# Performance work log

Hardware: AMD Instinct MI355X
Metric: run time of the kernel (lower is better)

Reference implementation:

```python
import jax, jax.numpy as jnp
import numpy as np

# Llama-7B FFN up-proj quantized with HQQ 4-bit, group_size=64, axis=0
OUT, IN, GS = 11008, 4096, 64
G = OUT * IN // GS  # 704512 groups


def setup_inputs() -> dict:
    key = jax.random.key(0)
    k1, k2, k3, k4, k5 = jax.random.split(key, 5)
    # packed 4-bit weights: two nibbles per byte, shape [GS//2, G]
    W_q = jax.random.randint(k1, (GS // 2, G), 0, 256, dtype=jnp.int32)
    # per-group scale (meta['scale'] = 1/scale from quantize) and zero
    scale = jax.random.uniform(k2, (1, G), jnp.float32, minval=1e-3, maxval=1e-2)
    zero = jax.random.uniform(k3, (1, G), jnp.float32, minval=0.0, maxval=15.0)
    # decode-style activations: 8 sequences, 1 token each
    x = jax.random.normal(k4, (8, 1, IN), dtype=jnp.float32)
    bias = jax.random.normal(k5, (OUT,), dtype=jnp.float32) * 0.01
    return {"W_q": W_q, "scale": scale, "zero": zero, "x": x, "bias": bias}


def reference(W_q, scale, zero, x, bias):
    # BitPack.unpack_4bit_u8: high nibble rows stacked on low nibble rows
    hi = (W_q >> 4) & 0xF
    lo = W_q & 0xF
    W_q_p = jnp.concatenate([hi, lo], axis=0).astype(x.dtype)  # [GS, G]
    # Quantizer.dequantize: (W_q_p - zero) * scale, reshape to weight shape
    W_r = ((W_q_p - zero) * scale).reshape(OUT, IN)  # [out, in]
    # torch.nn.functional.linear(x, W_r, bias)
    return jnp.einsum('bsi,oi->bso', x, W_r) + bias
```

## Files before the change

### kernel.cpp

```cpp
#include <hip/hip_runtime.h>


#define OUT_ 11008
#define IN_ 4096
#define G_ 704512
#define OC_ 172
#define KS 2
#define KC (IN_ / KS)
#define ITERS (KC / 256)

__global__ __launch_bounds__(256, 2)
void hqq_gemv(const int* __restrict__ Wq, const float* __restrict__ scale,
              const float* __restrict__ zero, const float* __restrict__ x,
              float* __restrict__ ws) {
    __shared__ float s_lds[KC];
    __shared__ float z_lds[KC];
    __shared__ float x_lds[8 * KC];

    const int lane = threadIdx.x;
    const int ty   = threadIdx.y;
    const int tid  = ty * 64 + lane;
    const int oc   = blockIdx.y;
    const int ks   = blockIdx.z;
    const int rq0  = blockIdx.x * 8 + ty * 2;

    const int kbase = ks * KC;
    const long gb = (long)oc * IN_ + kbase;

#pragma unroll
    for (int r = 0; r < KC / 1024; ++r) {
        const int off = r * 1024 + tid * 4;
        *(float4*)(s_lds + off) = *(const float4*)(scale + gb + off);
        *(float4*)(z_lds + off) = *(const float4*)(zero + gb + off);
    }
#pragma unroll
    for (int r = 0; r < 8 * KC / 1024; ++r) {
        const int off = r * 1024 + tid * 4;
        const int b = off >> 11;
        const int k = off & (KC - 1);
        *(float4*)(x_lds + off) = *(const float4*)(x + b * IN_ + kbase + k);
    }

    const int* __restrict__ wqA = Wq + (long)rq0 * G_ + gb;
    const int* __restrict__ wqB = wqA + G_;
    int4 qA[ITERS], qB[ITERS];
#pragma unroll
    for (int it = 0; it < ITERS; ++it) {
        qA[it] = *(const int4*)(wqA + it * 256 + lane * 4);
        qB[it] = *(const int4*)(wqB + it * 256 + lane * 4);
    }

    __syncthreads();

    float acc[4][8];
#pragma unroll
    for (int r = 0; r < 4; ++r)
#pragma unroll
        for (int b = 0; b < 8; ++b) acc[r][b] = 0.f;

#pragma unroll
    for (int it = 0; it < ITERS; ++it) {
        const int i = it * 256 + lane * 4;
        const float4 s4 = *(const float4*)(s_lds + i);
        const float4 z4 = *(const float4*)(z_lds + i);
        const float ss[4] = {s4.x, s4.y, s4.z, s4.w};
        const float zs[4] = {-z4.x * s4.x, -z4.y * s4.y, -z4.z * s4.z, -z4.w * s4.w};
        const int qsA[4] = {qA[it].x, qA[it].y, qA[it].z, qA[it].w};
        const int qsB[4] = {qB[it].x, qB[it].y, qB[it].z, qB[it].w};

        float w[4][4];
#pragma unroll
        for (int j = 0; j < 4; ++j) {
            w[0][j] = fmaf((float)((qsA[j] >> 4) & 0xF), ss[j], zs[j]);
            w[1][j] = fmaf((float)( qsA[j]       & 0xF), ss[j], zs[j]);
            w[2][j] = fmaf((float)((qsB[j] >> 4) & 0xF), ss[j], zs[j]);
            w[3][j] = fmaf((float)( qsB[j]       & 0xF), ss[j], zs[j]);
        }
#pragma unroll
        for (int b = 0; b < 8; ++b) {
            const float4 xb = *(const float4*)(x_lds + b * KC + i);
#pragma unroll
            for (int r = 0; r < 4; ++r) {
                float a = acc[r][b];
                a = fmaf(xb.x, w[r][0], a);
                a = fmaf(xb.y, w[r][1], a);
                a = fmaf(xb.z, w[r][2], a);
                a = fmaf(xb.w, w[r][3], a);
                acc[r][b] = a;
            }
        }
    }

#pragma unroll
    for (int r = 0; r < 4; ++r)
#pragma unroll
        for (int b = 0; b < 8; ++b) {
            float v = acc[r][b];
#pragma unroll
            for (int off = 32; off > 0; off >>= 1)
                v += __shfl_down(v, off, 64);
            acc[r][b] = v;
        }

    if (lane == 0) {
        const int o[4] = {rq0 * OC_ + oc, (rq0 + 32) * OC_ + oc,
                          (rq0 + 1) * OC_ + oc, (rq0 + 33) * OC_ + oc};
        float* __restrict__ wp = ws + (long)ks * 8 * OUT_;
#pragma unroll
        for (int r = 0; r < 4; ++r)
#pragma unroll
            for (int b = 0; b < 8; ++b)
                wp[b * OUT_ + o[r]] = acc[r][b];
    }
}

__global__ void hqq_reduce(const float* __restrict__ ws,
                           const float* __restrict__ bias,
                           float* __restrict__ out) {
    const int t = blockIdx.x * 256 + threadIdx.x;
    if (t >= 8 * OUT_) return;
    const int o = t % OUT_;
    float v = bias[o];
#pragma unroll
    for (int k = 0; k < KS; ++k) v += ws[k * 8 * OUT_ + t];
    out[t] = v;
}

extern "C" void kernel_launch(void* const* d_in, const int* in_sizes, int n_in,
                              void* d_out, int out_size, void* d_ws, size_t ws_size,
                              hipStream_t stream) {
    const int*   Wq    = (const int*)d_in[0];
    const float* scale = (const float*)d_in[1];
    const float* zero  = (const float*)d_in[2];
    const float* x     = (const float*)d_in[3];
    const float* bias  = (const float*)d_in[4];
    float* out = (float*)d_out;
    float* ws  = (float*)d_ws;

    dim3 grid(4, OC_, KS);
    dim3 block(64, 4);
    hqq_gemv<<<grid, block, 0, stream>>>(Wq, scale, zero, x, ws);
    hqq_reduce<<<(8 * OUT_ + 255) / 256, 256, 0, stream>>>(ws, bias, out);
}
```

Baseline: 152.0 us.

## Drop LDS staging, split K four ways, reduce partials through swizzled LDS

The GEMV no longer stages scale, zero and x in shared memory. It reads them straight from global memory, relying on cache, which removes the staging loads and the barrier before compute. The K dimension is now split four ways instead of two, with higher launch bounds, a flattened 1D grid, and block ordering that keeps one output chunk's K-splits adjacent. The per-wave shuffle reductions are replaced by a single XOR-swizzled LDS transpose reduction. In exchange, redundant global reads of x go to cache and twice as many partial sums go through the workspace.

```diff
diff --git a/kernel.cpp b/kernel.cpp
--- a/kernel.cpp
+++ b/kernel.cpp
@@ -5,41 +5,29 @@
 #define IN_ 4096
 #define G_ 704512
 #define OC_ 172
-#define KS 2
+#define KS 4
 #define KC (IN_ / KS)
 #define ITERS (KC / 256)
+#define SIB (OC_ * KS)
+#define NB (4 * SIB)
 
-__global__ __launch_bounds__(256, 2)
+__global__ __launch_bounds__(256, 4)
 void hqq_gemv(const int* __restrict__ Wq, const float* __restrict__ scale,
               const float* __restrict__ zero, const float* __restrict__ x,
               float* __restrict__ ws) {
-    __shared__ float s_lds[KC];
-    __shared__ float z_lds[KC];
-    __shared__ float x_lds[8 * KC];
+    __shared__ float red[128 * 64];
 
     const int lane = threadIdx.x;
     const int ty   = threadIdx.y;
-    const int tid  = ty * 64 + lane;
-    const int oc   = blockIdx.y;
-    const int ks   = blockIdx.z;
-    const int rq0  = blockIdx.x * 8 + ty * 2;
+    const int bid  = blockIdx.x;
+    const int bx   = bid / SIB;
+    const int rem  = bid % SIB;
+    const int oc   = rem >> 2;
+    const int ks   = rem & 3;
+    const int rq0  = bx * 8 + ty * 2;
 
     const int kbase = ks * KC;
-    const long gb = (long)oc * IN_ + kbase;
-
-#pragma unroll
-    for (int r = 0; r < KC / 1024; ++r) {
-        const int off = r * 1024 + tid * 4;
-        *(float4*)(s_lds + off) = *(const float4*)(scale + gb + off);
-        *(float4*)(z_lds + off) = *(const float4*)(zero + gb + off);
-    }
-#pragma unroll
-    for (int r = 0; r < 8 * KC / 1024; ++r) {
-        const int off = r * 1024 + tid * 4;
-        const int b = off >> 11;
-        const int k = off & (KC - 1);
-        *(float4*)(x_lds + off) = *(const float4*)(x + b * IN_ + kbase + k);
-    }
+    const int gb = oc * IN_ + kbase;
 
     const int* __restrict__ wqA = Wq + (long)rq0 * G_ + gb;
     const int* __restrict__ wqB = wqA + G_;
@@ -50,8 +38,6 @@
         qB[it] = *(const int4*)(wqB + it * 256 + lane * 4);
     }
 
-    __syncthreads();
-
     float acc[4][8];
 #pragma unroll
     for (int r = 0; r < 4; ++r)
@@ -61,8 +47,8 @@
 #pragma unroll
     for (int it = 0; it < ITERS; ++it) {
         const int i = it * 256 + lane * 4;
-        const float4 s4 = *(const float4*)(s_lds + i);
-        const float4 z4 = *(const float4*)(z_lds + i);
+        const float4 s4 = *(const float4*)(scale + gb + i);
+        const float4 z4 = *(const float4*)(zero + gb + i);
         const float ss[4] = {s4.x, s4.y, s4.z, s4.w};
         const float zs[4] = {-z4.x * s4.x, -z4.y * s4.y, -z4.z * s4.z, -z4.w * s4.w};
         const int qsA[4] = {qA[it].x, qA[it].y, qA[it].z, qA[it].w};
@@ -78,7 +64,7 @@
         }
 #pragma unroll
         for (int b = 0; b < 8; ++b) {
-            const float4 xb = *(const float4*)(x_lds + b * KC + i);
+            const float4 xb = *(const float4*)(x + b * IN_ + kbase + i);
 #pragma unroll
             for (int r = 0; r < 4; ++r) {
                 float a = acc[r][b];
@@ -91,26 +77,32 @@
         }
     }
 
+    const int obase = ty * 32;
 #pragma unroll
     for (int r = 0; r < 4; ++r)
 #pragma unroll
         for (int b = 0; b < 8; ++b) {
-            float v = acc[r][b];
+            const int o = obase + r * 8 + b;
+            red[o * 64 + (lane ^ ((o & 7) << 3))] = acc[r][b];
+        }
+    __syncthreads();
+
+    const int t = ty * 64 + lane;
+    if (t < 128) {
+        const int o = t;
+        const int c = (o & 7) << 3;
+        float s = 0.f;
 #pragma unroll
-            for (int off = 32; off > 0; off >>= 1)
-                v += __shfl_down(v, off, 64);
-            acc[r][b] = v;
+        for (int j = 0; j < 16; ++j) {
+            const float4 v = *(const float4*)(red + o * 64 + ((j * 4) ^ c));
+            s += (v.x + v.y) + (v.z + v.w);
         }
-
-    if (lane == 0) {
-        const int o[4] = {rq0 * OC_ + oc, (rq0 + 32) * OC_ + oc,
-                          (rq0 + 1) * OC_ + oc, (rq0 + 33) * OC_ + oc};
-        float* __restrict__ wp = ws + (long)ks * 8 * OUT_;
-#pragma unroll
-        for (int r = 0; r < 4; ++r)
-#pragma unroll
-            for (int b = 0; b < 8; ++b)
-                wp[b * OUT_ + o[r]] = acc[r][b];
+        const int w_  = o >> 5;
+        const int r   = (o >> 3) & 3;
+        const int b   = o & 7;
+        const int rq  = bx * 8 + w_ * 2 + (r >> 1);
+        const int row = rq + ((r & 1) ? 32 : 0);
+        ws[((long)ks * 8 + b) * OUT_ + row * OC_ + oc] = s;
     }
 }
 
@@ -137,7 +129,7 @@
     float* out = (float*)d_out;
     float* ws  = (float*)d_ws;
 
-    dim3 grid(4, OC_, KS);
+    dim3 grid(NB);
     dim3 block(64, 4);
     hqq_gemv<<<grid, block, 0, stream>>>(Wq, scale, zero, x, ws);
     hqq_reduce<<<(8 * OUT_ + 255) / 256, 256, 0, stream>>>(ws, bias, out);
```

Measured after the change: 152.2 us. About the same (+0.1%).
